# Performance work log

Measured on AMD Instinct MI355X. Metric: run time of the kernel, lower is better.

The kernel has to match this reference:

```python
import jax, jax.numpy as jnp
import numpy as np

NUM_HEADS = 8
SCALE_BASE = 512.0
GN_EPS = 1e-5


def rotate_every_two(x):
    x1 = x[..., ::2]
    x2 = x[..., 1::2]
    return jnp.stack([-x2, x1], axis=-1).reshape(x.shape)


def xpos_apply(x, downscale):
    # x: [B, T, D]; XPOS rotary with length-dependent scale (offset=0)
    L, D = x.shape[1], x.shape[2]
    half = D // 2
    scale_vec = (jnp.arange(0, D, 2, dtype=jnp.float32) + 0.4 * D) / (1.4 * D)  # [half]
    pos = jnp.arange(L, dtype=jnp.float32)
    scale = scale_vec[None, :] ** (pos[:, None] / SCALE_BASE)  # [L, half]
    inv_freq = 1.0 / (10000.0 ** (jnp.arange(half, dtype=jnp.float32) / half))
    sinusoid = pos[:, None] * inv_freq[None, :]  # [L, half]
    sin, cos = jnp.sin(sinusoid), jnp.cos(sinusoid)
    if downscale:
        scale = 1.0 / scale
    sin_s = jnp.repeat(sin * scale, 2, axis=-1)  # duplicate_interleave -> [L, D]
    cos_s = jnp.repeat(cos * scale, 2, axis=-1)
    return x * cos_s + rotate_every_two(x) * sin_s


def decay_mask_fn(T, num_heads):
    # gamma per head; decay stored as log(gamma) so mask = gamma^(i-j) on lower triangle
    s, e = np.log(1.0 / 32.0), np.log(1.0 / 512.0)
    gamma = 1.0 - jnp.exp(jnp.linspace(s, e, num_heads).astype(jnp.float32))
    log_decay = jnp.log(gamma)  # [H], negative
    idx = jnp.arange(T)
    expo = (idx[:, None] - idx[None, :]).astype(jnp.float32)  # i - j
    tri = (idx[:, None] >= idx[None, :])
    expo_safe = jnp.where(tri, expo, 0.0)
    mask = jnp.exp(log_decay[:, None, None] * expo_safe) * tri  # [H, T, T]
    scale = jnp.sqrt(mask.sum(axis=-1, keepdims=True))  # [H, T, 1]
    return mask / scale


def setup_inputs() -> dict:
    key = jax.random.key(0)
    ks = jax.random.split(key, 4)
    B, T, E = 2, 2048, 1024
    V = 2 * E
    return {
        "hidden_states": jax.random.normal(ks[0], (B, T, E), dtype=jnp.float32),
        "w_qkv": jax.random.normal(ks[1], (E, 2 * E + V), dtype=jnp.float32) * 0.02,
        "b_qkv": jnp.zeros((2 * E + V,), dtype=jnp.float32),
        "w_g": jax.random.normal(ks[2], (E, V), dtype=jnp.float32) * 0.02,
        "b_g": jnp.zeros((V,), dtype=jnp.float32),
        "w_p": jax.random.normal(ks[3], (V, E), dtype=jnp.float32) * 0.02,
        "b_p": jnp.zeros((E,), dtype=jnp.float32),
    }


def reference(hidden_states, w_qkv, b_qkv, w_g, b_g, w_p, b_p):
    B, T, E = hidden_states.shape
    H = NUM_HEADS
    V = 2 * E
    dk, dv = E // H, V // H

    qkv = hidden_states @ w_qkv + b_qkv
    q, k, v = qkv[..., :E], qkv[..., E:2 * E], qkv[..., 2 * E:]
    q = xpos_apply(q, downscale=False)
    k = xpos_apply(k, downscale=True)

    # split heads -> [B, H, T, d]
    q = q.reshape(B, T, H, dk).transpose(0, 2, 1, 3)
    k = k.reshape(B, T, H, dk).transpose(0, 2, 1, 3)
    v = v.reshape(B, T, H, dv).transpose(0, 2, 1, 3)

    mask = decay_mask_fn(T, H)  # [H, T, T]

    # parallel retention
    retention = jnp.einsum("bhid,bhjd->bhij", q, k) * (dk ** -0.5)
    retention = retention * mask[None]  # [B, H, T, T]
    out = jnp.einsum("bhij,bhjv->bhiv", retention, v)

    # current_kv = sum_j mask[h, -1, j] * k_j (x) v_j
    curr_kv = jnp.einsum("hj,bhjk,bhjv->bhkv", mask[:, -1, :], k, v)

    retention_out = out.transpose(0, 2, 1, 3).reshape(B, T, V)

    # GroupNorm(num_groups=H, affine=False) over v_dim channels
    g = retention_out.reshape(B * T, H, dv)
    mu = g.mean(axis=-1, keepdims=True)
    var = ((g - mu) ** 2).mean(axis=-1, keepdims=True)
    normed = ((g - mu) / jnp.sqrt(var + GN_EPS)).reshape(B, T, V)

    gated = jax.nn.silu(hidden_states @ w_g + b_g) * normed
    proj = gated @ w_p + b_p
    return proj, curr_kv
```

## Files before the change

kernel.cpp:

```cpp
#include <hip/hip_runtime.h>
#include <math.h>

#define BT      4096
#define T_SEQ   2048
#define E_DIM   1024
#define V_DIM   2048
#define DK      128
#define DV      256
#define QKV_LD  4096

typedef unsigned short ushort_t;
typedef __attribute__((ext_vector_type(8)))  short bf16x8;
typedef __attribute__((ext_vector_type(4)))  unsigned short u16x4;
typedef __attribute__((ext_vector_type(16))) float f32x16;

__device__ __forceinline__ void decay_params(int h, float& ld, float& gamma) {
    const float s0 = -3.4657359027997265f;
    const float e0 = -6.2383246250395092f;
    float lin = s0 + (e0 - s0) * ((float)h * (1.0f / 7.0f));
    gamma = 1.0f - expf(lin);
    ld = logf(gamma);
}

__device__ __forceinline__ short f2bf(float f) {
    unsigned u = __float_as_uint(f);
    unsigned r = (u + 0x7fffu + ((u >> 16) & 1u)) >> 16;
    return (short)r;
}
__device__ __forceinline__ float bf2f(ushort_t u) {
    return __uint_as_float((unsigned)u << 16);
}

__device__ __forceinline__ void async_copy16(void* lds, const void* g) {
    __builtin_amdgcn_global_load_lds(
        (const __attribute__((address_space(1))) unsigned int*)g,
        (__attribute__((address_space(3))) unsigned int*)lds, 16, 0, 0);
}

__global__ __launch_bounds__(256)
void f32_to_bf16_kernel(const float* __restrict__ in, ushort_t* __restrict__ out)
{
    int i = (blockIdx.x * 256 + threadIdx.x) * 8;
    float4 a = *(const float4*)&in[i];
    float4 b = *(const float4*)&in[i + 4];
    bf16x8 o;
    o[0] = f2bf(a.x); o[1] = f2bf(a.y); o[2] = f2bf(a.z); o[3] = f2bf(a.w);
    o[4] = f2bf(b.x); o[5] = f2bf(b.y); o[6] = f2bf(b.z); o[7] = f2bf(b.w);
    *(bf16x8*)&out[i] = o;
}

__global__ __launch_bounds__(256)
void transpose_w_kernel(const float* __restrict__ W, ushort_t* __restrict__ Wt,
                        int K, int N)
{
    __shared__ float tile[32][33];
    const int k0 = blockIdx.y * 32, n0 = blockIdx.x * 32;
    const int t = threadIdx.x;
    const int r = t >> 3, c = (t & 7) * 4;
    float4 v = *(const float4*)&W[(size_t)(k0 + r) * N + n0 + c];
    tile[r][c] = v.x; tile[r][c + 1] = v.y; tile[r][c + 2] = v.z; tile[r][c + 3] = v.w;
    __syncthreads();
    u16x4 o;
    o[0] = (ushort_t)f2bf(tile[c][r]);
    o[1] = (ushort_t)f2bf(tile[c + 1][r]);
    o[2] = (ushort_t)f2bf(tile[c + 2][r]);
    o[3] = (ushort_t)f2bf(tile[c + 3][r]);
    *(u16x4*)&Wt[(size_t)(n0 + r) * K + k0 + c] = o;
}

__global__ __launch_bounds__(512, 2)
void gemm256p8(const ushort_t* __restrict__ A,
               const ushort_t* __restrict__ Bt,
               const float* __restrict__ bias,
               float* __restrict__ C, int ldc, int nkt)
{
    __shared__ ushort_t As[2 * 16384];
    __shared__ ushort_t Bs[2 * 16384];

    const int tid = threadIdx.x;
    const int wid = tid >> 6, l = tid & 63;
    const int lc = l & 31, q = l >> 5;
    const int wr = wid >> 2, wc = wid & 3;
    const int m0 = blockIdx.y * 256, n0 = blockIdx.x * 256;

    const int sra = tid >> 3;
    const int spa = (tid & 7) ^ (sra & 7);
    const ushort_t* gA = A + (size_t)(m0 + sra) * 1024 + spa * 8;
    const int srb = tid >> 2;
    const int spb = (tid & 3) ^ ((srb >> 1) & 3);
    const ushort_t* gB = Bt + (size_t)(n0 + srb) * 1024 + spb * 8;
    const int da = tid * 8;

    int arow0 = (wr * 128 +  0 + lc) * 64;
    int arow1 = (wr * 128 + 32 + lc) * 64;
    int arow2 = (wr * 128 + 64 + lc) * 64;
    int arow3 = (wr * 128 + 96 + lc) * 64;
    int sk0 = ((0 * 2 + q) ^ (lc & 7)) * 8;
    int sk1 = ((1 * 2 + q) ^ (lc & 7)) * 8;
    int sk2 = ((2 * 2 + q) ^ (lc & 7)) * 8;
    int sk3 = ((3 * 2 + q) ^ (lc & 7)) * 8;
    int brow0 = (wc * 64 +  0 + lc) * 32;
    int brow1 = (wc * 64 + 32 + lc) * 32;
    int tk0 = ((0 + q) ^ ((lc >> 1) & 3)) * 8;
    int tk1 = ((2 + q) ^ ((lc >> 1) & 3)) * 8;
    int tk2 = 8192 + ((0 + q) ^ ((lc >> 1) & 3)) * 8;
    int tk3 = 8192 + ((2 + q) ^ ((lc >> 1) & 3)) * 8;

    f32x16 acc[4][2];
    #pragma unroll
    for (int mi = 0; mi < 4; ++mi)
        #pragma unroll
        for (int ni = 0; ni < 2; ++ni)
            #pragma unroll
            for (int e = 0; e < 16; ++e) acc[mi][ni][e] = 0.0f;

    async_copy16(&As[da],          gA);
    async_copy16(&As[8192 + da],   gA + 131072);
    async_copy16(&Bs[da],          gB);
    async_copy16(&Bs[4096 + da],   gB + 131072);
    async_copy16(&As[4096 + da],   gA + 65536);
    async_copy16(&As[12288 + da],  gA + 196608);
    async_copy16(&Bs[8192 + da],   gB + 32);
    async_copy16(&Bs[12288 + da],  gB + 131072 + 32);
    gA += 64; gB += 64;
    asm volatile("s_waitcnt vmcnt(0)" ::: "memory");
    __builtin_amdgcn_s_barrier();

    int cur = 0;
    for (int t = 0; t < nkt - 1; ++t) {
        const int cb = cur * 16384;
        const int nb = 16384 - cb;
        bf16x8 a00 = *(const bf16x8*)&As[cb + arow0 + sk0];
        bf16x8 a01 = *(const bf16x8*)&As[cb + arow0 + sk1];
        bf16x8 a10 = *(const bf16x8*)&As[cb + arow1 + sk0];
        bf16x8 a11 = *(const bf16x8*)&As[cb + arow1 + sk1];
        bf16x8 b00 = *(const bf16x8*)&Bs[cb + brow0 + tk0];
        bf16x8 b01 = *(const bf16x8*)&Bs[cb + brow0 + tk1];
        bf16x8 b10 = *(const bf16x8*)&Bs[cb + brow1 + tk0];
        bf16x8 b11 = *(const bf16x8*)&Bs[cb + brow1 + tk1];
        async_copy16(&As[nb + da],        gA);
        async_copy16(&As[nb + 8192 + da], gA + 131072);
        async_copy16(&Bs[nb + da],        gB);
        async_copy16(&Bs[nb + 4096 + da], gB + 131072);
        __builtin_amdgcn_s_barrier();
        asm volatile("s_waitcnt lgkmcnt(0)" ::: "memory");
        __builtin_amdgcn_s_setprio(1);
        acc[0][0] = __builtin_amdgcn_mfma_f32_32x32x16_bf16(a00, b00, acc[0][0], 0, 0, 0);
        acc[0][1] = __builtin_amdgcn_mfma_f32_32x32x16_bf16(a00, b10, acc[0][1], 0, 0, 0);
        acc[1][0] = __builtin_amdgcn_mfma_f32_32x32x16_bf16(a10, b00, acc[1][0], 0, 0, 0);
        acc[1][1] = __builtin_amdgcn_mfma_f32_32x32x16_bf16(a10, b10, acc[1][1], 0, 0, 0);
        acc[0][0] = __builtin_amdgcn_mfma_f32_32x32x16_bf16(a01, b01, acc[0][0], 0, 0, 0);
        acc[0][1] = __builtin_amdgcn_mfma_f32_32x32x16_bf16(a01, b11, acc[0][1], 0, 0, 0);
        acc[1][0] = __builtin_amdgcn_mfma_f32_32x32x16_bf16(a11, b01, acc[1][0], 0, 0, 0);
        acc[1][1] = __builtin_amdgcn_mfma_f32_32x32x16_bf16(a11, b11, acc[1][1], 0, 0, 0);
        __builtin_amdgcn_s_setprio(0);
        asm volatile("s_waitcnt vmcnt(6)" ::: "memory");
        __builtin_amdgcn_s_barrier();
        bf16x8 a20 = *(const bf16x8*)&As[cb + arow2 + sk0];
        bf16x8 a21 = *(const bf16x8*)&As[cb + arow2 + sk1];
        bf16x8 a30 = *(const bf16x8*)&As[cb + arow3 + sk0];
        bf16x8 a31 = *(const bf16x8*)&As[cb + arow3 + sk1];
        async_copy16(&As[nb + 4096 + da],  gA + 65536);
        async_copy16(&As[nb + 12288 + da], gA + 196608);
        __builtin_amdgcn_s_barrier();
        asm volatile("s_waitcnt lgkmcnt(0)" ::: "memory");
        __builtin_amdgcn_s_setprio(1);
// ... 62 lines not shown
        bf16x8 b00 = *(const bf16x8*)&Bs[cb + brow0 + tk0];
        bf16x8 b01 = *(const bf16x8*)&Bs[cb + brow0 + tk1];
        bf16x8 b10 = *(const bf16x8*)&Bs[cb + brow1 + tk0];
        bf16x8 b11 = *(const bf16x8*)&Bs[cb + brow1 + tk1];
        __builtin_amdgcn_s_barrier();
        asm volatile("s_waitcnt lgkmcnt(0)" ::: "memory");
        __builtin_amdgcn_s_setprio(1);
        acc[0][0] = __builtin_amdgcn_mfma_f32_32x32x16_bf16(a00, b00, acc[0][0], 0, 0, 0);
        acc[0][1] = __builtin_amdgcn_mfma_f32_32x32x16_bf16(a00, b10, acc[0][1], 0, 0, 0);
        acc[1][0] = __builtin_amdgcn_mfma_f32_32x32x16_bf16(a10, b00, acc[1][0], 0, 0, 0);
        acc[1][1] = __builtin_amdgcn_mfma_f32_32x32x16_bf16(a10, b10, acc[1][1], 0, 0, 0);
        acc[0][0] = __builtin_amdgcn_mfma_f32_32x32x16_bf16(a01, b01, acc[0][0], 0, 0, 0);
        acc[0][1] = __builtin_amdgcn_mfma_f32_32x32x16_bf16(a01, b11, acc[0][1], 0, 0, 0);
        acc[1][0] = __builtin_amdgcn_mfma_f32_32x32x16_bf16(a11, b01, acc[1][0], 0, 0, 0);
        acc[1][1] = __builtin_amdgcn_mfma_f32_32x32x16_bf16(a11, b11, acc[1][1], 0, 0, 0);
        __builtin_amdgcn_s_setprio(0);
        asm volatile("s_waitcnt vmcnt(2)" ::: "memory");
        __builtin_amdgcn_s_barrier();
        bf16x8 a20 = *(const bf16x8*)&As[cb + arow2 + sk0];
        bf16x8 a21 = *(const bf16x8*)&As[cb + arow2 + sk1];
        bf16x8 a30 = *(const bf16x8*)&As[cb + arow3 + sk0];
        bf16x8 a31 = *(const bf16x8*)&As[cb + arow3 + sk1];
        __builtin_amdgcn_s_barrier();
        asm volatile("s_waitcnt lgkmcnt(0)" ::: "memory");
        __builtin_amdgcn_s_setprio(1);
        acc[2][0] = __builtin_amdgcn_mfma_f32_32x32x16_bf16(a20, b00, acc[2][0], 0, 0, 0);
        acc[2][1] = __builtin_amdgcn_mfma_f32_32x32x16_bf16(a20, b10, acc[2][1], 0, 0, 0);
        acc[3][0] = __builtin_amdgcn_mfma_f32_32x32x16_bf16(a30, b00, acc[3][0], 0, 0, 0);
        acc[3][1] = __builtin_amdgcn_mfma_f32_32x32x16_bf16(a30, b10, acc[3][1], 0, 0, 0);
        acc[2][0] = __builtin_amdgcn_mfma_f32_32x32x16_bf16(a21, b01, acc[2][0], 0, 0, 0);
        acc[2][1] = __builtin_amdgcn_mfma_f32_32x32x16_bf16(a21, b11, acc[2][1], 0, 0, 0);
        acc[3][0] = __builtin_amdgcn_mfma_f32_32x32x16_bf16(a31, b01, acc[3][0], 0, 0, 0);
        acc[3][1] = __builtin_amdgcn_mfma_f32_32x32x16_bf16(a31, b11, acc[3][1], 0, 0, 0);
        __builtin_amdgcn_s_setprio(0);
        asm volatile("s_waitcnt vmcnt(0)" ::: "memory");
        __builtin_amdgcn_s_barrier();
        bf16x8 a02 = *(const bf16x8*)&As[cb + arow0 + sk2];
        bf16x8 a03 = *(const bf16x8*)&As[cb + arow0 + sk3];
        bf16x8 a12 = *(const bf16x8*)&As[cb + arow1 + sk2];
        bf16x8 a13 = *(const bf16x8*)&As[cb + arow1 + sk3];
        bf16x8 b02 = *(const bf16x8*)&Bs[cb + brow0 + tk2];
        bf16x8 b03 = *(const bf16x8*)&Bs[cb + brow0 + tk3];
        bf16x8 b12 = *(const bf16x8*)&Bs[cb + brow1 + tk2];
        bf16x8 b13 = *(const bf16x8*)&Bs[cb + brow1 + tk3];
        __builtin_amdgcn_s_barrier();
        asm volatile("s_waitcnt lgkmcnt(0)" ::: "memory");
        __builtin_amdgcn_s_setprio(1);
        acc[0][0] = __builtin_amdgcn_mfma_f32_32x32x16_bf16(a02, b02, acc[0][0], 0, 0, 0);
        acc[0][1] = __builtin_amdgcn_mfma_f32_32x32x16_bf16(a02, b12, acc[0][1], 0, 0, 0);
        acc[1][0] = __builtin_amdgcn_mfma_f32_32x32x16_bf16(a12, b02, acc[1][0], 0, 0, 0);
        acc[1][1] = __builtin_amdgcn_mfma_f32_32x32x16_bf16(a12, b12, acc[1][1], 0, 0, 0);
        acc[0][0] = __builtin_amdgcn_mfma_f32_32x32x16_bf16(a03, b03, acc[0][0], 0, 0, 0);
        acc[0][1] = __builtin_amdgcn_mfma_f32_32x32x16_bf16(a03, b13, acc[0][1], 0, 0, 0);
        acc[1][0] = __builtin_amdgcn_mfma_f32_32x32x16_bf16(a13, b03, acc[1][0], 0, 0, 0);
        acc[1][1] = __builtin_amdgcn_mfma_f32_32x32x16_bf16(a13, b13, acc[1][1], 0, 0, 0);
        __builtin_amdgcn_s_setprio(0);
        __builtin_amdgcn_s_barrier();
        bf16x8 a22 = *(const bf16x8*)&As[cb + arow2 + sk2];
        bf16x8 a23 = *(const bf16x8*)&As[cb + arow2 + sk3];
        bf16x8 a32 = *(const bf16x8*)&As[cb + arow3 + sk2];
        bf16x8 a33 = *(const bf16x8*)&As[cb + arow3 + sk3];
        asm volatile("s_waitcnt lgkmcnt(0)" ::: "memory");
        __builtin_amdgcn_s_setprio(1);
        acc[2][0] = __builtin_amdgcn_mfma_f32_32x32x16_bf16(a22, b02, acc[2][0], 0, 0, 0);
        acc[2][1] = __builtin_amdgcn_mfma_f32_32x32x16_bf16(a22, b12, acc[2][1], 0, 0, 0);
        acc[3][0] = __builtin_amdgcn_mfma_f32_32x32x16_bf16(a32, b02, acc[3][0], 0, 0, 0);
        acc[3][1] = __builtin_amdgcn_mfma_f32_32x32x16_bf16(a32, b12, acc[3][1], 0, 0, 0);
        acc[2][0] = __builtin_amdgcn_mfma_f32_32x32x16_bf16(a23, b03, acc[2][0], 0, 0, 0);
        acc[2][1] = __builtin_amdgcn_mfma_f32_32x32x16_bf16(a23, b13, acc[2][1], 0, 0, 0);
        acc[3][0] = __builtin_amdgcn_mfma_f32_32x32x16_bf16(a33, b03, acc[3][0], 0, 0, 0);
        acc[3][1] = __builtin_amdgcn_mfma_f32_32x32x16_bf16(a33, b13, acc[3][1], 0, 0, 0);
        __builtin_amdgcn_s_setprio(0);
    }

    #pragma unroll
    for (int ni = 0; ni < 2; ++ni) {
        const int col = n0 + wc * 64 + ni * 32 + lc;
        const float bb = bias[col];
        #pragma unroll
        for (int mi = 0; mi < 4; ++mi) {
            #pragma unroll
            for (int r = 0; r < 16; ++r) {
                const int row = m0 + wr * 128 + mi * 32 + (r & 3) + 8 * (r >> 2) + 4 * q;
                C[(size_t)row * ldc + col] = acc[mi][ni][r] + bb;
            }
        }
    }
}

__global__ __launch_bounds__(512)
void gemm_gate_p8(const ushort_t* __restrict__ A,
                  const ushort_t* __restrict__ Bt,
                  const float* __restrict__ bias,
                  ushort_t* __restrict__ C, int ldc,
                  const ushort_t* __restrict__ extra, int lde,
                  int nkt)
{
    __shared__ ushort_t As[2 * 8192];
    __shared__ ushort_t Bs[2 * 16384];

    const int tid = threadIdx.x;
    const int wid = tid >> 6, l = tid & 63;
    const int lc = l & 31, q = l >> 5;
    const int wr = wid >> 2, wc = wid & 3;
    const int m0 = blockIdx.y * 128, n0 = blockIdx.x * 256;

    const int sra = tid >> 3;
    const int spa = (tid & 7) ^ (sra & 7);
    const ushort_t* gA = A + (size_t)(m0 + sra) * 1024 + spa * 8;
    const int srb = tid >> 2;
    const int spb = (tid & 3) ^ ((srb >> 1) & 3);
    const ushort_t* gB = Bt + (size_t)(n0 + srb) * 1024 + spb * 8;
    const int da = tid * 8;

    int arow0 = (wr * 64 +  0 + lc) * 64;
    int arow1 = (wr * 64 + 32 + lc) * 64;
    int sk0 = ((0 * 2 + q) ^ (lc & 7)) * 8;
    int sk1 = ((1 * 2 + q) ^ (lc & 7)) * 8;
    int sk2 = ((2 * 2 + q) ^ (lc & 7)) * 8;
    int sk3 = ((3 * 2 + q) ^ (lc & 7)) * 8;
    int brow0 = (wc * 64 +  0 + lc) * 32;
    int brow1 = (wc * 64 + 32 + lc) * 32;
    int tk0 = ((0 + q) ^ ((lc >> 1) & 3)) * 8;
    int tk1 = ((2 + q) ^ ((lc >> 1) & 3)) * 8;
    int tk2 = 8192 + ((0 + q) ^ ((lc >> 1) & 3)) * 8;
    int tk3 = 8192 + ((2 + q) ^ ((lc >> 1) & 3)) * 8;

    f32x16 acc[2][2];
    #pragma unroll
    for (int mi = 0; mi < 2; ++mi)
        #pragma unroll
        for (int ni = 0; ni < 2; ++ni)
            #pragma unroll
            for (int e = 0; e < 16; ++e) acc[mi][ni][e] = 0.0f;

    async_copy16(&As[da],          gA);
    async_copy16(&As[4096 + da],   gA + 65536);
    async_copy16(&Bs[da],          gB);
    async_copy16(&Bs[4096 + da],   gB + 131072);
    async_copy16(&Bs[8192 + da],   gB + 32);
    async_copy16(&Bs[12288 + da],  gB + 131072 + 32);
    gA += 64; gB += 64;
    asm volatile("s_waitcnt vmcnt(0)" ::: "memory");
    __builtin_amdgcn_s_barrier();

    int cur = 0;
    for (int t = 0; t < nkt - 1; ++t) {
        const int ca = cur * 8192,  na = 8192 - ca;
        const int cb = cur * 16384, nb = 16384 - cb;
        bf16x8 a00 = *(const bf16x8*)&As[ca + arow0 + sk0];
        bf16x8 a01 = *(const bf16x8*)&As[ca + arow0 + sk1];
        bf16x8 a10 = *(const bf16x8*)&As[ca + arow1 + sk0];
        bf16x8 a11 = *(const bf16x8*)&As[ca + arow1 + sk1];
        bf16x8 b00 = *(const bf16x8*)&Bs[cb + brow0 + tk0];
        bf16x8 b01 = *(const bf16x8*)&Bs[cb + brow0 + tk1];
        bf16x8 b10 = *(const bf16x8*)&Bs[cb + brow1 + tk0];
        bf16x8 b11 = *(const bf16x8*)&Bs[cb + brow1 + tk1];
        async_copy16(&As[na + da],        gA);
        async_copy16(&As[na + 4096 + da], gA + 65536);
        async_copy16(&Bs[nb + da],        gB);
        async_copy16(&Bs[nb + 4096 + da], gB + 131072);
        __builtin_amdgcn_s_barrier();
        asm volatile("s_waitcnt lgkmcnt(0)" ::: "memory");
        __builtin_amdgcn_s_setprio(1);
        acc[0][0] = __builtin_amdgcn_mfma_f32_32x32x16_bf16(a00, b00, acc[0][0], 0, 0, 0);
        acc[0][1] = __builtin_amdgcn_mfma_f32_32x32x16_bf16(a00, b10, acc[0][1], 0, 0, 0);
        acc[1][0] = __builtin_amdgcn_mfma_f32_32x32x16_bf16(a10, b00, acc[1][0], 0, 0, 0);
        acc[1][1] = __builtin_amdgcn_mfma_f32_32x32x16_bf16(a10, b10, acc[1][1], 0, 0, 0);
        acc[0][0] = __builtin_amdgcn_mfma_f32_32x32x16_bf16(a01, b01, acc[0][0], 0, 0, 0);
        acc[0][1] = __builtin_amdgcn_mfma_f32_32x32x16_bf16(a01, b11, acc[0][1], 0, 0, 0);
        acc[1][0] = __builtin_amdgcn_mfma_f32_32x32x16_bf16(a11, b01, acc[1][0], 0, 0, 0);
        acc[1][1] = __builtin_amdgcn_mfma_f32_32x32x16_bf16(a11, b11, acc[1][1], 0, 0, 0);
        __builtin_amdgcn_s_setprio(0);
        asm volatile("s_waitcnt vmcnt(4)" ::: "memory");
        __builtin_amdgcn_s_barrier();
        bf16x8 a02 = *(const bf16x8*)&As[ca + arow0 + sk2];
        bf16x8 a03 = *(const bf16x8*)&As[ca + arow0 + sk3];
        bf16x8 a12 = *(const bf16x8*)&As[ca + arow1 + sk2];
        bf16x8 a13 = *(const bf16x8*)&As[ca + arow1 + sk3];
        bf16x8 b02 = *(const bf16x8*)&Bs[cb + brow0 + tk2];
        bf16x8 b03 = *(const bf16x8*)&Bs[cb + brow0 + tk3];
        bf16x8 b12 = *(const bf16x8*)&Bs[cb + brow1 + tk2];
        bf16x8 b13 = *(const bf16x8*)&Bs[cb + brow1 + tk3];
        async_copy16(&Bs[nb + 8192 + da],  gB + 32);
        async_copy16(&Bs[nb + 12288 + da], gB + 131072 + 32);
        gA += 64; gB += 64;
        __builtin_amdgcn_s_barrier();
        asm volatile("s_waitcnt lgkmcnt(0)" ::: "memory");
        __builtin_amdgcn_s_setprio(1);
        acc[0][0] = __builtin_amdgcn_mfma_f32_32x32x16_bf16(a02, b02, acc[0][0], 0, 0, 0);
        acc[0][1] = __builtin_amdgcn_mfma_f32_32x32x16_bf16(a02, b12, acc[0][1], 0, 0, 0);
        acc[1][0] = __builtin_amdgcn_mfma_f32_32x32x16_bf16(a12, b02, acc[1][0], 0, 0, 0);
        acc[1][1] = __builtin_amdgcn_mfma_f32_32x32x16_bf16(a12, b12, acc[1][1], 0, 0, 0);
        acc[0][0] = __builtin_amdgcn_mfma_f32_32x32x16_bf16(a03, b03, acc[0][0], 0, 0, 0);
        acc[0][1] = __builtin_amdgcn_mfma_f32_32x32x16_bf16(a03, b13, acc[0][1], 0, 0, 0);
        acc[1][0] = __builtin_amdgcn_mfma_f32_32x32x16_bf16(a13, b03, acc[1][0], 0, 0, 0);
        acc[1][1] = __builtin_amdgcn_mfma_f32_32x32x16_bf16(a13, b13, acc[1][1], 0, 0, 0);
        __builtin_amdgcn_s_setprio(0);
        asm volatile("s_waitcnt vmcnt(2)" ::: "memory");
        __builtin_amdgcn_s_barrier();
        cur ^= 1;
    }

    {
        const int ca = cur * 8192;
        const int cb = cur * 16384;
        bf16x8 a00 = *(const bf16x8*)&As[ca + arow0 + sk0];
        bf16x8 a01 = *(const bf16x8*)&As[ca + arow0 + sk1];
        bf16x8 a10 = *(const bf16x8*)&As[ca + arow1 + sk0];
        bf16x8 a11 = *(const bf16x8*)&As[ca + arow1 + sk1];
        bf16x8 b00 = *(const bf16x8*)&Bs[cb + brow0 + tk0];
        bf16x8 b01 = *(const bf16x8*)&Bs[cb + brow0 + tk1];
        bf16x8 b10 = *(const bf16x8*)&Bs[cb + brow1 + tk0];
        bf16x8 b11 = *(const bf16x8*)&Bs[cb + brow1 + tk1];
        __builtin_amdgcn_s_barrier();
        asm volatile("s_waitcnt lgkmcnt(0)" ::: "memory");
        __builtin_amdgcn_s_setprio(1);
        acc[0][0] = __builtin_amdgcn_mfma_f32_32x32x16_bf16(a00, b00, acc[0][0], 0, 0, 0);
        acc[0][1] = __builtin_amdgcn_mfma_f32_32x32x16_bf16(a00, b10, acc[0][1], 0, 0, 0);
        acc[1][0] = __builtin_amdgcn_mfma_f32_32x32x16_bf16(a10, b00, acc[1][0], 0, 0, 0);
        acc[1][1] = __builtin_amdgcn_mfma_f32_32x32x16_bf16(a10, b10, acc[1][1], 0, 0, 0);
        acc[0][0] = __builtin_amdgcn_mfma_f32_32x32x16_bf16(a01, b01, acc[0][0], 0, 0, 0);
        acc[0][1] = __builtin_amdgcn_mfma_f32_32x32x16_bf16(a01, b11, acc[0][1], 0, 0, 0);
        acc[1][0] = __builtin_amdgcn_mfma_f32_32x32x16_bf16(a11, b01, acc[1][0], 0, 0, 0);
        acc[1][1] = __builtin_amdgcn_mfma_f32_32x32x16_bf16(a11, b11, acc[1][1], 0, 0, 0);
        __builtin_amdgcn_s_setprio(0);
        asm volatile("s_waitcnt vmcnt(0)" ::: "memory");
        __builtin_amdgcn_s_barrier();
        bf16x8 a02 = *(const bf16x8*)&As[ca + arow0 + sk2];
        bf16x8 a03 = *(const bf16x8*)&As[ca + arow0 + sk3];
        bf16x8 a12 = *(const bf16x8*)&As[ca + arow1 + sk2];
        bf16x8 a13 = *(const bf16x8*)&As[ca + arow1 + sk3];
        bf16x8 b02 = *(const bf16x8*)&Bs[cb + brow0 + tk2];
        bf16x8 b03 = *(const bf16x8*)&Bs[cb + brow0 + tk3];
        bf16x8 b12 = *(const bf16x8*)&Bs[cb + brow1 + tk2];
        bf16x8 b13 = *(const bf16x8*)&Bs[cb + brow1 + tk3];
        asm volatile("s_waitcnt lgkmcnt(0)" ::: "memory");
        __builtin_amdgcn_s_setprio(1);
        acc[0][0] = __builtin_amdgcn_mfma_f32_32x32x16_bf16(a02, b02, acc[0][0], 0, 0, 0);
        acc[0][1] = __builtin_amdgcn_mfma_f32_32x32x16_bf16(a02, b12, acc[0][1], 0, 0, 0);
        acc[1][0] = __builtin_amdgcn_mfma_f32_32x32x16_bf16(a12, b02, acc[1][0], 0, 0, 0);
        acc[1][1] = __builtin_amdgcn_mfma_f32_32x32x16_bf16(a12, b12, acc[1][1], 0, 0, 0);
        acc[0][0] = __builtin_amdgcn_mfma_f32_32x32x16_bf16(a03, b03, acc[0][0], 0, 0, 0);
        acc[0][1] = __builtin_amdgcn_mfma_f32_32x32x16_bf16(a03, b13, acc[0][1], 0, 0, 0);
        acc[1][0] = __builtin_amdgcn_mfma_f32_32x32x16_bf16(a13, b03, acc[1][0], 0, 0, 0);
        acc[1][1] = __builtin_amdgcn_mfma_f32_32x32x16_bf16(a13, b13, acc[1][1], 0, 0, 0);
        __builtin_amdgcn_s_setprio(0);
    }

    #pragma unroll
    for (int ni = 0; ni < 2; ++ni) {
        const int col = n0 + wc * 64 + ni * 32 + lc;
        const float bb = bias[col];
        #pragma unroll
        for (int mi = 0; mi < 2; ++mi) {
            #pragma unroll
            for (int r = 0; r < 16; ++r) {
                const int row = m0 + wr * 64 + mi * 32 + (r & 3) + 8 * (r >> 2) + 4 * q;
                float val = acc[mi][ni][r] + bb;
                const float e = bf2f(extra[(size_t)row * lde + col]);
                val = val / (1.0f + expf(-val)) * e;
                C[(size_t)row * ldc + col] = (ushort_t)f2bf(val);
            }
        }
    }
}

__global__ __launch_bounds__(256)
void gemm_tm64(const ushort_t* __restrict__ A, int lda,
               const ushort_t* __restrict__ Bt, int ldb,
               const float* __restrict__ bias,
               float* __restrict__ C, int ldc, int nkt)
{
    __shared__ ushort_t As[3 * 64 * 32];
    __shared__ ushort_t Bs[3 * 128 * 32];

    const int tid = threadIdx.x;
    const int w  = tid >> 6, l = tid & 63;
    const int lc = l & 31, q = l >> 5;
    const int wr = w >> 1, wc = w & 1;
    const int m0 = blockIdx.y * 64, n0 = blockIdx.x * 128;

    const int rA = tid >> 2,          kcA = (tid & 3) ^ ((rA >> 1) & 3);
    const int rB1 = (256 + tid) >> 2, kcB1 = (tid & 3) ^ ((rB1 >> 1) & 3);
    const ushort_t* gA  = A  + (size_t)(m0 + rA)  * lda + kcA  * 8;
    const ushort_t* gB0 = Bt + (size_t)(n0 + rA)  * ldb + kcA  * 8;
    const ushort_t* gB1 = Bt + (size_t)(n0 + rB1) * ldb + kcB1 * 8;
    const int sA  = w * 512;
    const int sB0 = w * 512;
    const int sB1 = 2048 + w * 512;

    const int sl = (lc >> 1) & 3;
    int aoff[2], boff[2][2];
    #pragma unroll
    for (int ks = 0; ks < 2; ++ks) {
        const int kk = ks * 2 + q;
        const int mrow = wr * 32 + lc;
        aoff[ks] = (mrow * 4 + (kk ^ sl)) * 8;
        #pragma unroll
        for (int ni = 0; ni < 2; ++ni) {
            const int nrow = wc * 64 + ni * 32 + lc;
            boff[ni][ks] = (nrow * 4 + (kk ^ sl)) * 8;
        }
    }

    f32x16 acc[2];
    #pragma unroll
    for (int ni = 0; ni < 2; ++ni)
        #pragma unroll
        for (int e = 0; e < 16; ++e) acc[ni][e] = 0.0f;

    auto stage = [&](int ab, int bb) {
        async_copy16(&As[ab + sA], gA);
        async_copy16(&Bs[bb + sB0], gB0); async_copy16(&Bs[bb + sB1], gB1);
        gA += 32; gB0 += 32; gB1 += 32;
    };
    auto compute = [&](int ab, int bb) {
        bf16x8 a[2], b[2][2];
        #pragma unroll
        for (int ks = 0; ks < 2; ++ks) {
            a[ks] = *(const bf16x8*)&As[ab + aoff[ks]];
            b[0][ks] = *(const bf16x8*)&Bs[bb + boff[0][ks]];
            b[1][ks] = *(const bf16x8*)&Bs[bb + boff[1][ks]];
        }
        #pragma unroll
        for (int ks = 0; ks < 2; ++ks)
            #pragma unroll
            for (int ni = 0; ni < 2; ++ni)
                acc[ni] = __builtin_amdgcn_mfma_f32_32x32x16_bf16(
                    a[ks], b[ni][ks], acc[ni], 0, 0, 0);
    };

    stage(0, 0); stage(2048, 4096);
    int as_ = 4096, bs_ = 8192;
    int ac_ = 0,    bc_ = 0;
    for (int kt = 0; kt < nkt - 2; ++kt) {
        asm volatile("s_waitcnt vmcnt(3)" ::: "memory");
        __builtin_amdgcn_s_barrier();
        stage(as_, bs_);
        compute(ac_, bc_);
        as_ = ac_; bs_ = bc_;
        ac_ = (ac_ == 4096) ? 0 : ac_ + 2048;
        bc_ = (bc_ == 8192) ? 0 : bc_ + 4096;
    }
    asm volatile("s_waitcnt vmcnt(3)" ::: "memory");
    __builtin_amdgcn_s_barrier();
    compute(ac_, bc_);
    ac_ = (ac_ == 4096) ? 0 : ac_ + 2048;
    bc_ = (bc_ == 8192) ? 0 : bc_ + 4096;
    asm volatile("s_waitcnt vmcnt(0)" ::: "memory");
    __builtin_amdgcn_s_barrier();
    compute(ac_, bc_);

    #pragma unroll
    for (int ni = 0; ni < 2; ++ni) {
        const int col = n0 + wc * 64 + ni * 32 + lc;
        const float bb = bias[col];
        #pragma unroll
        for (int r = 0; r < 16; ++r) {
            const int row = m0 + wr * 32 + (r & 3) + 8 * (r >> 2) + 4 * q;
            C[(size_t)row * ldc + col] = acc[ni][r] + bb;
        }
    }
}

__global__ __launch_bounds__(256)
void qk_prep(const float* __restrict__ qkv,
             ushort_t* __restrict__ qh, ushort_t* __restrict__ kh)
{
    const int row = blockIdx.x;
    const int t = threadIdx.x;
    const int b = row >> 11, trow = row & (T_SEQ - 1);
    const bool isK = t >= 128;
    const int col0 = (t & 127) * 8;
    const int h = col0 >> 7, d = col0 & 127;

    float ld, gamma;
    decay_params(h, ld, gamma);
    const float gsc = __expf(isK ? -ld * (float)(trow & 63) : ld * (float)(trow & 63));

    const float* src = qkv + (size_t)row * QKV_LD + (isK ? E_DIM : 0) + col0;
    float4 x0 = *(const float4*)src;
    float4 x1 = *(const float4*)(src + 4);
    float xv[8] = {x0.x, x0.y, x0.z, x0.w, x1.x, x1.y, x1.z, x1.w};

    const float tf = (float)trow * (1.0f / 512.0f);
    bf16x8 o;
    #pragma unroll
    for (int pi = 0; pi < 4; ++pi) {
        const int ip = col0 / 2 + pi;
        float sv = (2.0f * (float)ip + 409.6f) * (1.0f / 1433.6f);
        float e = __logf(sv) * tf;
        if (isK) e = -e;
        float sc = __expf(e);
        float invf = __expf((float)ip * -0.017988946038999563f);
        float sn, cs;
        sincosf((float)trow * invf, &sn, &cs);
        float c = cs * sc * gsc, s = sn * sc * gsc;
        float a = xv[2 * pi], bb = xv[2 * pi + 1];
        o[2 * pi]     = f2bf(a * c - bb * s);
        o[2 * pi + 1] = f2bf(bb * c + a * s);
    }
    ushort_t* dst = (isK ? kh : qh) + ((size_t)(b * 8 + h) * T_SEQ + trow) * 128 + d;
    *(bf16x8*)dst = o;
}

__global__ __launch_bounds__(256)
void v_transpose(const float* __restrict__ qkv, ushort_t* __restrict__ vt)
{
    __shared__ float tile[32][33];
    const int j0 = blockIdx.x * 32;
    const int zz = blockIdx.y;
    const int bh = zz >> 3, v0 = (zz & 7) * 32;
    const int b = bh >> 3, h = bh & 7;
    const int t = threadIdx.x;
    const int r = t >> 3, c = (t & 7) * 4;

    float4 x = *(const float4*)(qkv + (size_t)(b * T_SEQ + j0 + r) * QKV_LD
                                + 2 * E_DIM + h * DV + v0 + c);
    tile[r][c] = x.x; tile[r][c+1] = x.y; tile[r][c+2] = x.z; tile[r][c+3] = x.w;
    __syncthreads();
    u16x4 o;
    o[0] = (ushort_t)f2bf(tile[c][r]);
    o[1] = (ushort_t)f2bf(tile[c + 1][r]);
    o[2] = (ushort_t)f2bf(tile[c + 2][r]);
    o[3] = (ushort_t)f2bf(tile[c + 3][r]);
    *(u16x4*)&vt[((size_t)bh * 256 + v0 + r) * T_SEQ + j0 + c] = o;
}

__global__ __launch_bounds__(256)
void kt2_kernel(const ushort_t* __restrict__ kh, ushort_t* __restrict__ kt2)
{
    __shared__ ushort_t tile[32][40];
    const int j0 = blockIdx.x * 32;
    const int zz = blockIdx.y;
    const int bh = zz >> 2, k0 = (zz & 3) * 32;
    const int t = threadIdx.x;
    const int r = t >> 3, c = (t & 7) * 4;
    float ld, gamma; decay_params(bh & 7, ld, gamma);
    const float g63 = expf(ld * 63.0f);
    *(u16x4*)&tile[r][c] = *(const u16x4*)&kh[((size_t)bh * T_SEQ + j0 + r) * 128 + k0 + c];
    __syncthreads();
    u16x4 o;
    o[0] = (ushort_t)f2bf(bf2f(tile[c][r])     * g63);
    o[1] = (ushort_t)f2bf(bf2f(tile[c + 1][r]) * g63);
    o[2] = (ushort_t)f2bf(bf2f(tile[c + 2][r]) * g63);
    o[3] = (ushort_t)f2bf(bf2f(tile[c + 3][r]) * g63);
    *(u16x4*)&kt2[((size_t)bh * 128 + k0 + r) * T_SEQ + j0 + c] = o;
}

__global__ __launch_bounds__(256)
void chunk_kv(const ushort_t* __restrict__ vt, const ushort_t* __restrict__ kt2,
              ushort_t* __restrict__ Abuf)
{
    const int c = blockIdx.x;
    const int bh = blockIdx.y;
    const int tid = threadIdx.x;
    const int w = tid >> 6, l = tid & 63, lc = l & 31, q = l >> 5;
    const int j0 = c * 64;

    f32x16 acc[2][4];
    #pragma unroll
    for (int mi = 0; mi < 2; ++mi)
        #pragma unroll
        for (int ni = 0; ni < 4; ++ni)
            #pragma unroll
            for (int e = 0; e < 16; ++e) acc[mi][ni][e] = 0.0f;

    #pragma unroll
    for (int ks = 0; ks < 4; ++ks) {
        bf16x8 a[2], bfr[4];
        #pragma unroll
        for (int mi = 0; mi < 2; ++mi)
            a[mi] = *(const bf16x8*)(vt + ((size_t)bh * 256 + w * 64 + mi * 32 + lc) * T_SEQ
                                     + j0 + ks * 16 + q * 8);
        #pragma unroll
        for (int ni = 0; ni < 4; ++ni)
            bfr[ni] = *(const bf16x8*)(kt2 + ((size_t)bh * 128 + ni * 32 + lc) * T_SEQ
                                       + j0 + ks * 16 + q * 8);
        #pragma unroll
        for (int mi = 0; mi < 2; ++mi)
            #pragma unroll
            for (int ni = 0; ni < 4; ++ni)
                acc[mi][ni] = __builtin_amdgcn_mfma_f32_32x32x16_bf16(
                    a[mi], bfr[ni], acc[mi][ni], 0, 0, 0);
    }

    ushort_t* ab = Abuf + (size_t)(bh * 32 + c) * 256 * 128;
    #pragma unroll
    for (int mi = 0; mi < 2; ++mi)
        #pragma unroll
        for (int ni = 0; ni < 4; ++ni)
            #pragma unroll
            for (int r = 0; r < 16; ++r) {
                const int v = w * 64 + mi * 32 + (r & 3) + 8 * (r >> 2) + 4 * q;
                const int k = ni * 32 + lc;
                ab[(size_t)v * 128 + k] = (ushort_t)f2bf(acc[mi][ni][r]);
            }
}

__global__ __launch_bounds__(256)
void scan_state(const ushort_t* __restrict__ Abuf, ushort_t* __restrict__ St,
                float* __restrict__ ckv)
{
    const int blk = blockIdx.x;
    const int bh = blk >> 7, sub = blk & 127;
    const int tid = threadIdx.x;
    const int v = sub * 2 + (tid >> 7), k = tid & 127;

    float ld, gamma;
    decay_params(bh & 7, ld, gamma);
    const float g64 = expf(ld * 64.0f);

    const size_t base = ((size_t)bh * 32 * 256 + v) * 128 + k;
    const size_t cstr = 256 * 128;
    float s = 0.0f;
    for (int c = 0; c < 32; ++c) {
        const size_t off = base + (size_t)c * cstr;
        St[off] = (ushort_t)f2bf(gamma * s);
        s = g64 * s + bf2f(Abuf[off]);
    }
    const float inv_scale = rsqrtf((1.0f - expf(ld * (float)T_SEQ)) / (1.0f - gamma));
    ckv[((size_t)bh * 128 + k) * 256 + v] = s * inv_scale;
}

__global__ __launch_bounds__(64)
void retention_chunk(const ushort_t* __restrict__ qh,
                     const ushort_t* __restrict__ kh,
                     const ushort_t* __restrict__ vt,
                     const ushort_t* __restrict__ St,
                     ushort_t* __restrict__ normed)
{
    const int it = blockIdx.x;
    const int bh = blockIdx.y;
    const int b = bh >> 3, h = bh & 7;
    const int c = it >> 1, w = it & 1;
    const int l = threadIdx.x, lc = l & 31, q = l >> 5;
    const int i0 = it * 32;
    const size_t bhT = (size_t)bh * T_SEQ;

    float ld, gamma;
    decay_params(h, ld, gamma);

    bf16x8 qf[8];
    {
        const ushort_t* qp = qh + (bhT + i0 + lc) * 128 + q * 8;
        #pragma unroll
        for (int c8 = 0; c8 < 8; ++c8)
            qf[c8] = *(const bf16x8*)(qp + c8 * 16);
    }

    f32x16 acc[8];
    #pragma unroll
    for (int vg = 0; vg < 8; ++vg)
        #pragma unroll
        for (int e = 0; e < 16; ++e) acc[vg][e] = 0.0f;

    if (c > 0) {
        const ushort_t* sp = St + ((size_t)(bh * 32 + c) * 256 + lc) * 128 + q * 8;
        #pragma unroll
        for (int vg = 0; vg < 8; ++vg) {
            const ushort_t* spv = sp + (size_t)vg * 32 * 128;
            #pragma unroll
            for (int ks = 0; ks < 8; ++ks) {
                bf16x8 sb = *(const bf16x8*)(spv + ks * 16);
                acc[vg] = __builtin_amdgcn_mfma_f32_32x32x16_bf16(
                    qf[ks], sb, acc[vg], 0, 0, 0);
            }
        }
    }

    for (int jt2 = 0; jt2 <= w; ++jt2) {
        const int j0 = c * 64 + jt2 * 32;

        f32x16 s;
        #pragma unroll
        for (int e = 0; e < 16; ++e) s[e] = 0.0f;
        const ushort_t* kp = kh + (bhT + j0 + lc) * 128 + q * 8;
        #pragma unroll
        for (int c8 = 0; c8 < 8; ++c8) {
            bf16x8 ka = *(const bf16x8*)(kp + c8 * 16);
            s = __builtin_amdgcn_mfma_f32_32x32x16_bf16(ka, qf[c8], s, 0, 0, 0);
        }

        float sv[16];
        #pragma unroll
        for (int r = 0; r < 16; ++r) {
            float val = s[r];
            if (jt2 == w) {
                int jr_ = (r & 3) + 8 * (r >> 2) + 4 * q;
                val = (jr_ <= lc) ? val : 0.0f;
            }
            sv[r] = val;
        }

        bf16x8 pa0, pa1;
        #pragma unroll
        for (int e = 0; e < 4; ++e) {
            float t1 = __shfl_xor(sv[e + 4], 32);
            float t0 = __shfl_xor(sv[e], 32);
            pa0[e]     = f2bf(q ? t1 : sv[e]);
            pa0[e + 4] = f2bf(q ? sv[e + 4] : t0);
            float t3 = __shfl_xor(sv[e + 12], 32);
            float t2 = __shfl_xor(sv[e + 8], 32);
            pa1[e]     = f2bf(q ? t3 : sv[e + 8]);
            pa1[e + 4] = f2bf(q ? sv[e + 12] : t2);
        }

        #pragma unroll
        for (int vg = 0; vg < 8; ++vg) {
            const ushort_t* vp = vt + ((size_t)bh * 256 + vg * 32 + lc) * T_SEQ + j0 + q * 8;
            bf16x8 vb0 = *(const bf16x8*)vp;
            bf16x8 vb1 = *(const bf16x8*)(vp + 16);
            acc[vg] = __builtin_amdgcn_mfma_f32_32x32x16_bf16(pa0, vb0, acc[vg], 0, 0, 0);
            acc[vg] = __builtin_amdgcn_mfma_f32_32x32x16_bf16(pa1, vb1, acc[vg], 0, 0, 0);
        }
    }

    #pragma unroll
    for (int r = 0; r < 16; ++r) {
        const int il = (r & 3) + 8 * (r >> 2) + 4 * q;
        const int i  = i0 + il;
        float denom = (1.0f - expf(ld * (float)(i + 1))) / (1.0f - gamma);
        float fs = 0.08838834764831845f * rsqrtf(denom);
        float vals[8];
        float a1 = 0.0f, a2 = 0.0f;
        #pragma unroll
        for (int vg = 0; vg < 8; ++vg) {
            float x = acc[vg][r] * fs;
            vals[vg] = x;
            a1 += x; a2 += x * x;
        }
        a1 += __shfl_xor(a1, 1);  a2 += __shfl_xor(a2, 1);
        a1 += __shfl_xor(a1, 2);  a2 += __shfl_xor(a2, 2);
        a1 += __shfl_xor(a1, 4);  a2 += __shfl_xor(a2, 4);
        a1 += __shfl_xor(a1, 8);  a2 += __shfl_xor(a2, 8);
        a1 += __shfl_xor(a1, 16); a2 += __shfl_xor(a2, 16);
        float mu = a1 * (1.0f / 256.0f);
        float var = a2 * (1.0f / 256.0f) - mu * mu;
        float rs = rsqrtf(var + 1e-5f);
        ushort_t* op = normed + ((size_t)(b * T_SEQ + i)) * V_DIM + h * DV + lc;
        #pragma unroll
        for (int vg = 0; vg < 8; ++vg)
            op[vg * 32] = (ushort_t)f2bf((vals[vg] - mu) * rs);
    }
}

extern "C" void kernel_launch(void* const* d_in, const int* in_sizes, int n_in,
                              void* d_out, int out_size, void* d_ws, size_t ws_size,
                              hipStream_t stream)
{
    const float* hs    = (const float*)d_in[0];
    const float* w_qkv = (const float*)d_in[1];
    const float* b_qkv = (const float*)d_in[2];
    const float* w_g   = (const float*)d_in[3];
    const float* b_g   = (const float*)d_in[4];
    const float* w_p   = (const float*)d_in[5];
    const float* b_p   = (const float*)d_in[6];
    float* out = (float*)d_out;

    const size_t MB = 1024 * 1024;
    float*    qkv      = (float*)d_ws;
    ushort_t* Abuf     = (ushort_t*)d_ws;
    ushort_t* normed   = (ushort_t*)d_ws;
    ushort_t* Stbuf    = (ushort_t*)((char*)d_ws + 32 * MB);
    ushort_t* gated_bf = (ushort_t*)((char*)d_ws + 32 * MB);
    ushort_t* wg_t     = (ushort_t*)((char*)d_ws + 56 * MB);
    ushort_t* wp_t     = (ushort_t*)((char*)d_ws + 60 * MB);
    ushort_t* qh       = (ushort_t*)((char*)d_ws + 64 * MB);
    ushort_t* vt       = (ushort_t*)((char*)d_ws + 72 * MB);
    ushort_t* wqkv_t   = (ushort_t*)((char*)d_ws + 88 * MB);
    ushort_t* kh       = (ushort_t*)((char*)d_ws + 88 * MB);
    ushort_t* hs_bf    = (ushort_t*)d_out;
    ushort_t* kt2      = (ushort_t*)((char*)d_out + 8 * MB);
    float*    ckv_out  = out + (size_t)BT * E_DIM;

    f32_to_bf16_kernel<<<dim3(2048), 256, 0, stream>>>(hs, hs_bf);
    transpose_w_kernel<<<dim3(128, 32), 256, 0, stream>>>(w_qkv, wqkv_t, E_DIM, 4096);

    gemm256p8<<<dim3(16, 16), 512, 0, stream>>>(
        hs_bf, wqkv_t, b_qkv, qkv, QKV_LD, E_DIM / 64);

    qk_prep<<<dim3(BT), 256, 0, stream>>>(qkv, qh, kh);
    v_transpose<<<dim3(64, 128), 256, 0, stream>>>(qkv, vt);
    kt2_kernel<<<dim3(64, 64), 256, 0, stream>>>(kh, kt2);

    chunk_kv<<<dim3(32, 16), 256, 0, stream>>>(vt, kt2, Abuf);
    scan_state<<<dim3(2048), 256, 0, stream>>>(Abuf, Stbuf, ckv_out);
    retention_chunk<<<dim3(64, 16), 64, 0, stream>>>(qh, kh, vt, Stbuf, normed);

    transpose_w_kernel<<<dim3(64, 32), 256, 0, stream>>>(w_g, wg_t, E_DIM, V_DIM);
    transpose_w_kernel<<<dim3(32, 64), 256, 0, stream>>>(w_p, wp_t, V_DIM, E_DIM);

    gemm_gate_p8<<<dim3(8, 32), 512, 0, stream>>>(
        hs_bf, wg_t, b_g, gated_bf, V_DIM, normed, V_DIM, E_DIM / 64);

    gemm_tm64<<<dim3(8, 64), 256, 0, stream>>>(
        gated_bf, V_DIM, wp_t, V_DIM, b_p, out, E_DIM, V_DIM / 32);
}
```

Before: 310.2 us.

## Store QKV in bf16, fuse gating into retention, add XCD-aware tile remap

The QKV GEMM now writes bf16 instead of fp32, which halves the intermediate's write and read traffic for qk_prep and v_transpose. The gate GEMM runs earlier and stores only silu(x@Wg+b), and the multiply with the normalized retention output moves into the retention kernel's epilogue, so the separate normed buffer round-trip goes away. All three GEMMs also get an XCD-aware block remapping meant to improve L2 locality. Rounding QKV to bf16 before the xpos rotation adds precision loss, and the workspace buffers are reshuffled to reuse overlapping regions.

```diff
diff --git a/kernel.cpp b/kernel.cpp
--- a/kernel.cpp
+++ b/kernel.cpp
@@ -7,7 +7,6 @@
 #define V_DIM   2048
 #define DK      128
 #define DV      256
-#define QKV_LD  4096
 
 typedef unsigned short ushort_t;
 typedef __attribute__((ext_vector_type(8)))  short bf16x8;
@@ -35,6 +34,15 @@
     __builtin_amdgcn_global_load_lds(
         (const __attribute__((address_space(1))) unsigned int*)g,
         (__attribute__((address_space(3))) unsigned int*)lds, 16, 0, 0);
+}
+
+__device__ __forceinline__ void xcd_tile(int& bx, int& by) {
+    const int nwgx = gridDim.x;
+    const int nwg  = nwgx * gridDim.y;
+    int bid = blockIdx.y * nwgx + blockIdx.x;
+    bid = (bid & 7) * (nwg >> 3) + (bid >> 3);
+    bx = bid % nwgx;
+    by = bid / nwgx;
 }
 
 __global__ __launch_bounds__(256)
@@ -72,7 +80,7 @@
 void gemm256p8(const ushort_t* __restrict__ A,
                const ushort_t* __restrict__ Bt,
                const float* __restrict__ bias,
-               float* __restrict__ C, int ldc, int nkt)
+               ushort_t* __restrict__ C, int ldc, int nkt)
 {
     __shared__ ushort_t As[2 * 16384];
     __shared__ ushort_t Bs[2 * 16384];
@@ -81,7 +89,8 @@
     const int wid = tid >> 6, l = tid & 63;
     const int lc = l & 31, q = l >> 5;
     const int wr = wid >> 2, wc = wid & 3;
-    const int m0 = blockIdx.y * 256, n0 = blockIdx.x * 256;
+    int bx, by; xcd_tile(bx, by);
+    const int m0 = by * 256, n0 = bx * 256;
 
     const int sra = tid >> 3;
     const int spa = (tid & 7) ^ (sra & 7);
@@ -310,7 +319,7 @@
             #pragma unroll
             for (int r = 0; r < 16; ++r) {
                 const int row = m0 + wr * 128 + mi * 32 + (r & 3) + 8 * (r >> 2) + 4 * q;
-                C[(size_t)row * ldc + col] = acc[mi][ni][r] + bb;
+                C[(size_t)row * ldc + col] = (ushort_t)f2bf(acc[mi][ni][r] + bb);
             }
         }
     }
@@ -321,7 +330,6 @@
                   const ushort_t* __restrict__ Bt,
                   const float* __restrict__ bias,
                   ushort_t* __restrict__ C, int ldc,
-                  const ushort_t* __restrict__ extra, int lde,
                   int nkt)
 {
     __shared__ ushort_t As[2 * 8192];
@@ -331,7 +339,8 @@
     const int wid = tid >> 6, l = tid & 63;
     const int lc = l & 31, q = l >> 5;
     const int wr = wid >> 2, wc = wid & 3;
-    const int m0 = blockIdx.y * 128, n0 = blockIdx.x * 256;
+    int bx, by; xcd_tile(bx, by);
+    const int m0 = by * 128, n0 = bx * 256;
 
     const int sra = tid >> 3;
     const int spa = (tid & 7) ^ (sra & 7);
@@ -486,8 +495,7 @@
             for (int r = 0; r < 16; ++r) {
                 const int row = m0 + wr * 64 + mi * 32 + (r & 3) + 8 * (r >> 2) + 4 * q;
                 float val = acc[mi][ni][r] + bb;
-                const float e = bf2f(extra[(size_t)row * lde + col]);
-                val = val / (1.0f + expf(-val)) * e;
+                val = val / (1.0f + expf(-val));
                 C[(size_t)row * ldc + col] = (ushort_t)f2bf(val);
             }
         }
@@ -507,7 +515,8 @@
     const int w  = tid >> 6, l = tid & 63;
     const int lc = l & 31, q = l >> 5;
     const int wr = w >> 1, wc = w & 1;
-    const int m0 = blockIdx.y * 64, n0 = blockIdx.x * 128;
+    int bx, by; xcd_tile(bx, by);
+    const int m0 = by * 64, n0 = bx * 128;
 
     const int rA = tid >> 2,          kcA = (tid & 3) ^ ((rA >> 1) & 3);
     const int rB1 = (256 + tid) >> 2, kcB1 = (tid & 3) ^ ((rB1 >> 1) & 3);
@@ -593,7 +602,7 @@
 }
 
 __global__ __launch_bounds__(256)
-void qk_prep(const float* __restrict__ qkv,
+void qk_prep(const ushort_t* __restrict__ qkvb,
              ushort_t* __restrict__ qh, ushort_t* __restrict__ kh)
 {
     const int row = blockIdx.x;
@@ -607,10 +616,11 @@
     decay_params(h, ld, gamma);
     const float gsc = __expf(isK ? -ld * (float)(trow & 63) : ld * (float)(trow & 63));
 
-    const float* src = qkv + (size_t)row * QKV_LD + (isK ? E_DIM : 0) + col0;
-    float4 x0 = *(const float4*)src;
-    float4 x1 = *(const float4*)(src + 4);
-    float xv[8] = {x0.x, x0.y, x0.z, x0.w, x1.x, x1.y, x1.z, x1.w};
+    const ushort_t* src = qkvb + (size_t)row * 4096 + (isK ? E_DIM : 0) + col0;
+    bf16x8 xv8 = *(const bf16x8*)src;
+    float xv[8];
+    #pragma unroll
+    for (int p = 0; p < 8; ++p) xv[p] = bf2f((ushort_t)xv8[p]);
 
     const float tf = (float)trow * (1.0f / 512.0f);
     bf16x8 o;
@@ -634,9 +644,9 @@
 }
 
 __global__ __launch_bounds__(256)
-void v_transpose(const float* __restrict__ qkv, ushort_t* __restrict__ vt)
-{
-    __shared__ float tile[32][33];
+void v_transpose(const ushort_t* __restrict__ qkvb, ushort_t* __restrict__ vt)
+{
+    __shared__ ushort_t tile[32][40];
     const int j0 = blockIdx.x * 32;
     const int zz = blockIdx.y;
     const int bh = zz >> 3, v0 = (zz & 7) * 32;
@@ -644,15 +654,14 @@
     const int t = threadIdx.x;
     const int r = t >> 3, c = (t & 7) * 4;
 
-    float4 x = *(const float4*)(qkv + (size_t)(b * T_SEQ + j0 + r) * QKV_LD
-                                + 2 * E_DIM + h * DV + v0 + c);
-    tile[r][c] = x.x; tile[r][c+1] = x.y; tile[r][c+2] = x.z; tile[r][c+3] = x.w;
+    *(u16x4*)&tile[r][c] = *(const u16x4*)(qkvb + (size_t)(b * T_SEQ + j0 + r) * 4096
+                                           + 2 * E_DIM + h * DV + v0 + c);
     __syncthreads();
     u16x4 o;
-    o[0] = (ushort_t)f2bf(tile[c][r]);
-    o[1] = (ushort_t)f2bf(tile[c + 1][r]);
-    o[2] = (ushort_t)f2bf(tile[c + 2][r]);
-    o[3] = (ushort_t)f2bf(tile[c + 3][r]);
+    o[0] = tile[c][r];
+    o[1] = tile[c + 1][r];
+    o[2] = tile[c + 2][r];
+    o[3] = tile[c + 3][r];
     *(u16x4*)&vt[((size_t)bh * 256 + v0 + r) * T_SEQ + j0 + c] = o;
 }
 
@@ -745,8 +754,9 @@
     float s = 0.0f;
     for (int c = 0; c < 32; ++c) {
         const size_t off = base + (size_t)c * cstr;
+        const float a = bf2f(Abuf[off]);
         St[off] = (ushort_t)f2bf(gamma * s);
-        s = g64 * s + bf2f(Abuf[off]);
+        s = g64 * s + a;
     }
     const float inv_scale = rsqrtf((1.0f - expf(ld * (float)T_SEQ)) / (1.0f - gamma));
     ckv[((size_t)bh * 128 + k) * 256 + v] = s * inv_scale;
@@ -757,7 +767,8 @@
                      const ushort_t* __restrict__ kh,
                      const ushort_t* __restrict__ vt,
                      const ushort_t* __restrict__ St,
-                     ushort_t* __restrict__ normed)
+                     const ushort_t* __restrict__ grw,
+                     ushort_t* __restrict__ gated)
 {
     const int it = blockIdx.x;
     const int bh = blockIdx.y;
@@ -867,10 +878,14 @@
         float mu = a1 * (1.0f / 256.0f);
         float var = a2 * (1.0f / 256.0f) - mu * mu;
         float rs = rsqrtf(var + 1e-5f);
-        ushort_t* op = normed + ((size_t)(b * T_SEQ + i)) * V_DIM + h * DV + lc;
-        #pragma unroll
-        for (int vg = 0; vg < 8; ++vg)
-            op[vg * 32] = (ushort_t)f2bf((vals[vg] - mu) * rs);
+        const size_t ob = ((size_t)(b * T_SEQ + i)) * V_DIM + h * DV + lc;
+        ushort_t* op = gated + ob;
+        const ushort_t* gp = grw + ob;
+        #pragma unroll
+        for (int vg = 0; vg < 8; ++vg) {
+            float g = bf2f(gp[vg * 32]);
+            op[vg * 32] = (ushort_t)f2bf((vals[vg] - mu) * rs * g);
+        }
     }
 }
 
@@ -888,13 +903,13 @@
     float* out = (float*)d_out;
 
     const size_t MB = 1024 * 1024;
-    float*    qkv      = (float*)d_ws;
+    ushort_t* qkv_bf   = (ushort_t*)d_ws;
     ushort_t* Abuf     = (ushort_t*)d_ws;
-    ushort_t* normed   = (ushort_t*)d_ws;
-    ushort_t* Stbuf    = (ushort_t*)((char*)d_ws + 32 * MB);
-    ushort_t* gated_bf = (ushort_t*)((char*)d_ws + 32 * MB);
-    ushort_t* wg_t     = (ushort_t*)((char*)d_ws + 56 * MB);
-    ushort_t* wp_t     = (ushort_t*)((char*)d_ws + 60 * MB);
+    ushort_t* Stbuf    = (ushort_t*)d_ws;
+    ushort_t* wp_t     = (ushort_t*)d_ws;
+    ushort_t* gate_raw = (ushort_t*)((char*)d_ws + 32 * MB);
+    ushort_t* gated_bf = (ushort_t*)((char*)d_ws + 48 * MB);
+    ushort_t* wg_t     = (ushort_t*)((char*)d_ws + 64 * MB);
     ushort_t* qh       = (ushort_t*)((char*)d_ws + 64 * MB);
     ushort_t* vt       = (ushort_t*)((char*)d_ws + 72 * MB);
     ushort_t* wqkv_t   = (ushort_t*)((char*)d_ws + 88 * MB);
@@ -904,25 +919,24 @@
     float*    ckv_out  = out + (size_t)BT * E_DIM;
 
     f32_to_bf16_kernel<<<dim3(2048), 256, 0, stream>>>(hs, hs_bf);
+    transpose_w_kernel<<<dim3(64, 32), 256, 0, stream>>>(w_g, wg_t, E_DIM, V_DIM);
     transpose_w_kernel<<<dim3(128, 32), 256, 0, stream>>>(w_qkv, wqkv_t, E_DIM, 4096);
 
+    gemm_gate_p8<<<dim3(8, 32), 512, 0, stream>>>(
+        hs_bf, wg_t, b_g, gate_raw, V_DIM, E_DIM / 64);
+
     gemm256p8<<<dim3(16, 16), 512, 0, stream>>>(
-        hs_bf, wqkv_t, b_qkv, qkv, QKV_LD, E_DIM / 64);
-
-    qk_prep<<<dim3(BT), 256, 0, stream>>>(qkv, qh, kh);
-    v_transpose<<<dim3(64, 128), 256, 0, stream>>>(qkv, vt);
+        hs_bf, wqkv_t, b_qkv, qkv_bf, 4096, E_DIM / 64);
+
+    qk_prep<<<dim3(BT), 256, 0, stream>>>(qkv_bf, qh, kh);
+    v_transpose<<<dim3(64, 128), 256, 0, stream>>>(qkv_bf, vt);
     kt2_kernel<<<dim3(64, 64), 256, 0, stream>>>(kh, kt2);
 
     chunk_kv<<<dim3(32, 16), 256, 0, stream>>>(vt, kt2, Abuf);
     scan_state<<<dim3(2048), 256, 0, stream>>>(Abuf, Stbuf, ckv_out);
-    retention_chunk<<<dim3(64, 16), 64, 0, stream>>>(qh, kh, vt, Stbuf, normed);
-
-    transpose_w_kernel<<<dim3(64, 32), 256, 0, stream>>>(w_g, wg_t, E_DIM, V_DIM);
+    retention_chunk<<<dim3(64, 16), 64, 0, stream>>>(qh, kh, vt, Stbuf, gate_raw, gated_bf);
+
     transpose_w_kernel<<<dim3(32, 64), 256, 0, stream>>>(w_p, wp_t, V_DIM, E_DIM);
-
-    gemm_gate_p8<<<dim3(8, 32), 512, 0, stream>>>(
-        hs_bf, wg_t, b_g, gated_bf, V_DIM, normed, V_DIM, E_DIM / 64);
-
     gemm_tm64<<<dim3(8, 64), 256, 0, stream>>>(
         gated_bf, V_DIM, wp_t, V_DIM, b_p, out, E_DIM, V_DIM / 32);
 }
```

Measured after the change: 296.4 us. 1.05x faster.
